# Optimization experiments

Hardware: AMD Instinct MI355X
Metric: run time of the kernel (lower is better)

## Reference

```python
import jax, jax.numpy as jnp
import numpy as np

DIM_U1 = 20
DIM_U2 = 20
DZ = 6
BATCH = 4096


def _mlp(x, Wa, ba, Wb, bb, Wc, bc, Wd, bd):
    h = jax.nn.relu(x @ Wa + ba)
    h = jax.nn.relu(h @ Wb + bb)
    h = jax.nn.relu(h @ Wc + bc)
    return h @ Wd + bd


def setup_inputs() -> dict:
    key = jax.random.key(0)
    ks = jax.random.split(key, 9)

    def lin(k, fan_in, fan_out):
        k1, k2 = jax.random.split(k)
        lim = 1.0 / np.sqrt(fan_in)
        W = jax.random.uniform(k1, (fan_in, fan_out), minval=-lim, maxval=lim, dtype=jnp.float32)
        b = jax.random.uniform(k2, (fan_out,), minval=-lim, maxval=lim, dtype=jnp.float32)
        return W, b

    d = {"x": jax.random.normal(ks[0], (BATCH, DIM_U1), dtype=jnp.float32)}
    dims1 = [(3, 16), (16, 32), (32, 16), (16, 1 + DZ * 3)]
    dims2 = [(3, 16), (16, 32), (32, 16), (16, DZ + 5 * DZ * DZ)]
    names = ["a", "b", "c", "d"]
    for j, (fi, fo) in enumerate(dims1):
        W, b = lin(ks[1 + j], fi, fo)
        d["W1" + names[j]] = W
        d["b1" + names[j]] = b
    for j, (fi, fo) in enumerate(dims2):
        W, b = lin(ks[5 + j], fi, fo)
        d["W2" + names[j]] = W
        d["b2" + names[j]] = b
    return d


def reference(x, W1a, b1a, W1b, b1b, W1c, b1c, W1d, b1d,
              W2a, b2a, W2b, b2b, W2c, b2c, W2d, b2d):
    B = x.shape[0]
    # gather local neighbor triples: [B, dim_u1, 3]
    idx = (jnp.arange(DIM_U1)[:, None] + jnp.arange(-1, 2)[None, :]) % DIM_U1
    xl = x[:, idx]
    out1 = _mlp(xl, W1a, b1a, W1b, b1b, W1c, b1c, W1d, b1d)  # [B, 20, 19]
    out2 = _mlp(xl, W2a, b2a, W2b, b2b, W2c, b2c, W2d, b2d)  # [B, 20, 186]

    f1 = out1[:, :, :1]  # [B, 20, 1]

    # banded scatter for g1: [B, dim_u1, dz*dim_u2]
    rows1 = jnp.arange(DIM_U1)[:, None]
    cols1 = (jnp.arange(3 * DZ)[None, :] + (jnp.arange(DIM_U1)[:, None] - 1) * DZ) % (DZ * DIM_U2)
    g1 = jnp.zeros((B, DIM_U1, DZ * DIM_U2), x.dtype).at[:, rows1, cols1].set(out1[:, :, 1:])

    f2 = out2[:, :, :DZ].reshape(B, DZ * DIM_U2, 1)

    # banded scatter for g2: [B, dz*dim_u2, dz*dim_u2]
    rows2 = jnp.arange(DZ * DIM_U2)[:, None]
    base = (jnp.arange(5 * DZ)[None, :] + (jnp.arange(DIM_U2)[:, None] - 2) * DZ) % (DZ * DIM_U2)  # [20, 30]
    cols2 = jnp.repeat(base, DZ, axis=0)  # [120, 30]
    vals2 = out2[:, :, DZ:].reshape(B, DZ * DIM_U2, 5 * DZ)
    g2 = jnp.zeros((B, DZ * DIM_U2, DZ * DIM_U2), x.dtype).at[:, rows2, cols2].set(vals2)

    return (f1, g1, f2, g2)
```

## Files before the change

### kernel.cpp

```cpp
#include <hip/hip_runtime.h>

typedef unsigned short u16;
typedef unsigned int   u32;

#define U 20

struct Ptrs { const float* p[16]; };

static __device__ __forceinline__ float bf2f(u16 h) {
    u32 u = ((u32)h) << 16;
    float f;
    __builtin_memcpy(&f, &u, 4);
    return f;
}

static __device__ __forceinline__ u16 f2bf(float f) {
    u32 u;
    __builtin_memcpy(&u, &f, 4);
    u32 lsb = (u >> 16) & 1u;
    u += 0x7fffu + lsb;
    return (u16)(u >> 16);
}

static __device__ __forceinline__ float gr(float f) { return bf2f(f2bf(f)); }

__launch_bounds__(256)
__global__ void fused(const float* __restrict__ x, Ptrs pt,
                      float* __restrict__ out, int B, int total) {
    const int tid = threadIdx.x;
    const int t   = blockIdx.x * 256 + tid;

    const size_t g1_off = (size_t)B * 20;
    const size_t f2_off = (size_t)B * 2420;
    const size_t g2_off = (size_t)B * 2540;

    {
        int t0  = blockIdx.x * 256;
        int n_t = total - t0; if (n_t > 256) n_t = 256; if (n_t < 0) n_t = 0;
        float4 z4; z4.x = z4.y = z4.z = z4.w = 0.f;
        float4* z1 = reinterpret_cast<float4*>(out + g1_off + (size_t)t0 * 120);
        int c1 = n_t * 30;
        for (int idx = tid; idx < c1; idx += 256) z1[idx] = z4;
        float4* z2 = reinterpret_cast<float4*>(out + g2_off + (size_t)t0 * 720);
        int c2 = n_t * 180;
        for (int idx = tid; idx < c2; idx += 256) z2[idx] = z4;
    }
    __syncthreads();
    if (t >= total) return;

    const int b = t / U;
    const int i = t - b * U;

    const float* W1a = pt.p[0];  const float* b1a = pt.p[1];
    const float* W1b = pt.p[2];  const float* b1b = pt.p[3];
    const float* W1c = pt.p[4];  const float* b1c = pt.p[5];
    const float* W1d = pt.p[6];  const float* b1d = pt.p[7];
    const float* W2a = pt.p[8];  const float* b2a = pt.p[9];
    const float* W2b = pt.p[10]; const float* b2b = pt.p[11];
    const float* W2c = pt.p[12]; const float* b2c = pt.p[13];
    const float* W2d = pt.p[14]; const float* b2d = pt.p[15];

    float* g1row  = out + g1_off + (size_t)t * 120;
    float* g2rows = out + g2_off + (size_t)t * 720;

    const float* xb = x + (size_t)b * U;
    int im = (i == 0)     ? U - 1 : i - 1;
    int ip = (i == U - 1) ? 0     : i + 1;
    float v0 = xb[im], v1 = xb[i], v2 = xb[ip];

    float h1[16], h2[32], h3[16];

    #pragma unroll
    for (int n = 0; n < 16; n++)
        h1[n] = fmaxf(b1a[n] + v0 * W1a[n] + v1 * W1a[16 + n] + v2 * W1a[32 + n], 0.f);

    #pragma unroll
    for (int n = 0; n < 32; n++) h2[n] = b1b[n];
    #pragma unroll
    for (int k = 0; k < 16; k++) {
        float hk = h1[k];
        #pragma unroll
        for (int n = 0; n < 32; n++) h2[n] += hk * W1b[k * 32 + n];
    }
    #pragma unroll
    for (int n = 0; n < 32; n++) h2[n] = fmaxf(h2[n], 0.f);

    #pragma unroll
    for (int n = 0; n < 16; n++) h3[n] = b1c[n];
    #pragma unroll
    for (int k = 0; k < 32; k++) {
        float hk = h2[k];
        #pragma unroll
        for (int n = 0; n < 16; n++) h3[n] += hk * W1c[k * 16 + n];
    }
    #pragma unroll
    for (int n = 0; n < 16; n++) h3[n] = fmaxf(h3[n], 0.f);

    {
        float o1[19];
        #pragma unroll
        for (int n = 0; n < 19; n++) o1[n] = b1d[n];
        #pragma unroll
        for (int k = 0; k < 16; k++) {
            float hk = h3[k];
            #pragma unroll
            for (int n = 0; n < 19; n++) o1[n] += hk * W1d[k * 19 + n];
        }
        out[t] = gr(o1[0]);
        #pragma unroll
        for (int j = 0; j < 3; j++) {
            int cc = i - 1 + j;
            if (cc < 0)  cc += U;
            if (cc >= U) cc -= U;
            float2* d = reinterpret_cast<float2*>(g1row + cc * 6);
            #pragma unroll
            for (int m = 0; m < 3; m++) {
                float2 v; v.x = gr(o1[1 + j * 6 + 2 * m]);
                          v.y = gr(o1[1 + j * 6 + 2 * m + 1]);
                d[m] = v;
            }
        }
    }

    #pragma unroll
    for (int n = 0; n < 16; n++)
        h1[n] = fmaxf(b2a[n] + v0 * W2a[n] + v1 * W2a[16 + n] + v2 * W2a[32 + n], 0.f);

    #pragma unroll
    for (int n = 0; n < 32; n++) h2[n] = b2b[n];
    #pragma unroll
    for (int k = 0; k < 16; k++) {
        float hk = h1[k];
        #pragma unroll
        for (int n = 0; n < 32; n++) h2[n] += hk * W2b[k * 32 + n];
    }
    #pragma unroll
    for (int n = 0; n < 32; n++) h2[n] = fmaxf(h2[n], 0.f);

    #pragma unroll
    for (int n = 0; n < 16; n++) h3[n] = b2c[n];
    #pragma unroll
    for (int k = 0; k < 32; k++) {
        float hk = h2[k];
        #pragma unroll
        for (int n = 0; n < 16; n++) h3[n] += hk * W2c[k * 16 + n];
    }
    #pragma unroll
    for (int n = 0; n < 16; n++) h3[n] = fmaxf(h3[n], 0.f);

    {
        float o2a[6];
        #pragma unroll
        for (int n = 0; n < 6; n++) o2a[n] = b2d[n];
        #pragma unroll
        for (int k = 0; k < 16; k++) {
            float hk = h3[k];
            #pragma unroll
            for (int n = 0; n < 6; n++) o2a[n] += hk * W2d[k * 186 + n];
        }
        float2* d = reinterpret_cast<float2*>(out + f2_off + (size_t)t * 6);
        #pragma unroll
        for (int m = 0; m < 3; m++) {
            float2 v; v.x = gr(o2a[2 * m]); v.y = gr(o2a[2 * m + 1]);
            d[m] = v;
        }
    }

    for (int z = 0; z < 6; z++) {
        float o2[30];
        #pragma unroll
        for (int n = 0; n < 30; n++) o2[n] = b2d[6 + z * 30 + n];
        #pragma unroll
        for (int k = 0; k < 16; k++) {
            float hk = h3[k];
            #pragma unroll
            for (int n = 0; n < 30; n++) o2[n] += hk * W2d[k * 186 + 6 + z * 30 + n];
        }
        float* row = g2rows + z * 120;
        #pragma unroll
        for (int j = 0; j < 5; j++) {
            int cc = i - 2 + j;
            if (cc < 0)  cc += U;
            if (cc >= U) cc -= U;
            float2* d = reinterpret_cast<float2*>(row + cc * 6);
            #pragma unroll
            for (int m = 0; m < 3; m++) {
                float2 v; v.x = gr(o2[j * 6 + 2 * m]);
                          v.y = gr(o2[j * 6 + 2 * m + 1]);
                d[m] = v;
            }
        }
    }
}

extern "C" void kernel_launch(void* const* d_in, const int* in_sizes, int n_in,
                              void* d_out, int out_size, void* d_ws, size_t ws_size,
                              hipStream_t stream) {
    const float* x = (const float*)d_in[0];
    Ptrs pt;
    for (int a = 0; a < 16; a++) pt.p[a] = (const float*)d_in[1 + a];

    int total = in_sizes[0];
    int B = total / U;

    int blocks = (total + 255) / 256;
    fused<<<blocks, 256, 0, stream>>>(x, pt, (float*)d_out, B, total);
}
```

Before: 389.6 us.

## Shrink blocks to one wavefront, overlap zero-fill with MLP, drop bf16 rounding

Blocks go from 256 threads to 64. The barrier after the zero-fill now comes after the first MLP's compute, so the zero-fill stores overlap with arithmetic instead of stalling before it. The bf16 round-trip on every output value is removed and fp32 results are stored directly. This cuts the ALU work of the rounding and lets more small blocks run concurrently, but it changes numerics relative to the earlier bf16-rounded outputs.

```diff
diff --git a/kernel.cpp b/kernel.cpp
--- a/kernel.cpp
+++ b/kernel.cpp
@@ -1,55 +1,34 @@
 #include <hip/hip_runtime.h>
-
-typedef unsigned short u16;
-typedef unsigned int   u32;
 
 #define U 20
 
 struct Ptrs { const float* p[16]; };
 
-static __device__ __forceinline__ float bf2f(u16 h) {
-    u32 u = ((u32)h) << 16;
-    float f;
-    __builtin_memcpy(&f, &u, 4);
-    return f;
-}
-
-static __device__ __forceinline__ u16 f2bf(float f) {
-    u32 u;
-    __builtin_memcpy(&u, &f, 4);
-    u32 lsb = (u >> 16) & 1u;
-    u += 0x7fffu + lsb;
-    return (u16)(u >> 16);
-}
-
-static __device__ __forceinline__ float gr(float f) { return bf2f(f2bf(f)); }
-
-__launch_bounds__(256)
+__launch_bounds__(64)
 __global__ void fused(const float* __restrict__ x, Ptrs pt,
                       float* __restrict__ out, int B, int total) {
     const int tid = threadIdx.x;
-    const int t   = blockIdx.x * 256 + tid;
+    const int t   = blockIdx.x * 64 + tid;
 
     const size_t g1_off = (size_t)B * 20;
     const size_t f2_off = (size_t)B * 2420;
     const size_t g2_off = (size_t)B * 2540;
 
     {
-        int t0  = blockIdx.x * 256;
-        int n_t = total - t0; if (n_t > 256) n_t = 256; if (n_t < 0) n_t = 0;
+        int t0  = blockIdx.x * 64;
+        int n_t = total - t0; if (n_t > 64) n_t = 64; if (n_t < 0) n_t = 0;
         float4 z4; z4.x = z4.y = z4.z = z4.w = 0.f;
         float4* z1 = reinterpret_cast<float4*>(out + g1_off + (size_t)t0 * 120);
         int c1 = n_t * 30;
-        for (int idx = tid; idx < c1; idx += 256) z1[idx] = z4;
+        for (int idx = tid; idx < c1; idx += 64) z1[idx] = z4;
         float4* z2 = reinterpret_cast<float4*>(out + g2_off + (size_t)t0 * 720);
         int c2 = n_t * 180;
-        for (int idx = tid; idx < c2; idx += 256) z2[idx] = z4;
+        for (int idx = tid; idx < c2; idx += 64) z2[idx] = z4;
     }
-    __syncthreads();
-    if (t >= total) return;
 
-    const int b = t / U;
-    const int i = t - b * U;
+    const bool live = (t < total);
+    const int b = live ? (t / U) : 0;
+    const int i = live ? (t - b * U) : 0;
 
     const float* W1a = pt.p[0];  const float* b1a = pt.p[1];
     const float* W1b = pt.p[2];  const float* b1b = pt.p[3];
@@ -60,15 +39,13 @@
     const float* W2c = pt.p[12]; const float* b2c = pt.p[13];
     const float* W2d = pt.p[14]; const float* b2d = pt.p[15];
 
-    float* g1row  = out + g1_off + (size_t)t * 120;
-    float* g2rows = out + g2_off + (size_t)t * 720;
-
     const float* xb = x + (size_t)b * U;
     int im = (i == 0)     ? U - 1 : i - 1;
     int ip = (i == U - 1) ? 0     : i + 1;
     float v0 = xb[im], v1 = xb[i], v2 = xb[ip];
 
     float h1[16], h2[32], h3[16];
+    float o1[19];
 
     #pragma unroll
     for (int n = 0; n < 16; n++)
@@ -96,29 +73,32 @@
     #pragma unroll
     for (int n = 0; n < 16; n++) h3[n] = fmaxf(h3[n], 0.f);
 
-    {
-        float o1[19];
+    #pragma unroll
+    for (int n = 0; n < 19; n++) o1[n] = b1d[n];
+    #pragma unroll
+    for (int k = 0; k < 16; k++) {
+        float hk = h3[k];
         #pragma unroll
-        for (int n = 0; n < 19; n++) o1[n] = b1d[n];
+        for (int n = 0; n < 19; n++) o1[n] += hk * W1d[k * 19 + n];
+    }
+
+    __syncthreads();
+    if (!live) return;
+
+    float* g1row  = out + g1_off + (size_t)t * 120;
+    float* g2rows = out + g2_off + (size_t)t * 720;
+
+    out[t] = o1[0];
+    #pragma unroll
+    for (int j = 0; j < 3; j++) {
+        int cc = i - 1 + j;
+        if (cc < 0)  cc += U;
+        if (cc >= U) cc -= U;
+        float2* d = reinterpret_cast<float2*>(g1row + cc * 6);
         #pragma unroll
-        for (int k = 0; k < 16; k++) {
-            float hk = h3[k];
-            #pragma unroll
-            for (int n = 0; n < 19; n++) o1[n] += hk * W1d[k * 19 + n];
-        }
-        out[t] = gr(o1[0]);
-        #pragma unroll
-        for (int j = 0; j < 3; j++) {
-            int cc = i - 1 + j;
-            if (cc < 0)  cc += U;
-            if (cc >= U) cc -= U;
-            float2* d = reinterpret_cast<float2*>(g1row + cc * 6);
-            #pragma unroll
-            for (int m = 0; m < 3; m++) {
-                float2 v; v.x = gr(o1[1 + j * 6 + 2 * m]);
-                          v.y = gr(o1[1 + j * 6 + 2 * m + 1]);
-                d[m] = v;
-            }
+        for (int m = 0; m < 3; m++) {
+            float2 v; v.x = o1[1 + j * 6 + 2 * m]; v.y = o1[1 + j * 6 + 2 * m + 1];
+            d[m] = v;
         }
     }
 
@@ -161,7 +141,7 @@
         float2* d = reinterpret_cast<float2*>(out + f2_off + (size_t)t * 6);
         #pragma unroll
         for (int m = 0; m < 3; m++) {
-            float2 v; v.x = gr(o2a[2 * m]); v.y = gr(o2a[2 * m + 1]);
+            float2 v; v.x = o2a[2 * m]; v.y = o2a[2 * m + 1];
             d[m] = v;
         }
     }
@@ -185,8 +165,7 @@
             float2* d = reinterpret_cast<float2*>(row + cc * 6);
             #pragma unroll
             for (int m = 0; m < 3; m++) {
-                float2 v; v.x = gr(o2[j * 6 + 2 * m]);
-                          v.y = gr(o2[j * 6 + 2 * m + 1]);
+                float2 v; v.x = o2[j * 6 + 2 * m]; v.y = o2[j * 6 + 2 * m + 1];
                 d[m] = v;
             }
         }
@@ -203,6 +182,6 @@
     int total = in_sizes[0];
     int B = total / U;
 
-    int blocks = (total + 255) / 256;
-    fused<<<blocks, 256, 0, stream>>>(x, pt, (float*)d_out, B, total);
+    int blocks = (total + 63) / 64;
+    fused<<<blocks, 64, 0, stream>>>(x, pt, (float*)d_out, B, total);
 }
```

After: 390.8 us. Within noise of the previous version (+0.3%).
